# Optimization experiments

Hardware: AMD Instinct MI355X
Metric: run time of the kernel (lower is better)

The kernel has to match this reference:

```python
import jax, jax.numpy as jnp
import numpy as np

N_NODES = 50000
N_EDGES = 800000
D_IN = 128
D_HID = 128
D_OUT = 128
BN_EPS = 1e-5


def _lin_params(key, d_out, d_in, bias=True):
    k1, k2 = jax.random.split(key)
    s = 1.0 / np.sqrt(d_in)
    W = jax.random.uniform(k1, (d_out, d_in), jnp.float32, -s, s)
    b = jax.random.uniform(k2, (d_out,), jnp.float32, -s, s) if bias else None
    return W, b


def setup_inputs() -> dict:
    key = jax.random.key(0)
    ks = jax.random.split(key, 10)
    x = jax.random.normal(ks[0], (N_NODES, D_IN), jnp.float32)
    edge_index = jax.random.randint(ks[1], (2, N_EDGES), 0, N_NODES, jnp.int32)
    Wl0, bl0 = _lin_params(ks[2], D_HID, D_IN)
    Wr0, _ = _lin_params(ks[3], D_HID, D_IN, bias=False)
    Wl1, bl1 = _lin_params(ks[4], D_HID, D_HID)
    Wr1, _ = _lin_params(ks[5], D_HID, D_HID, bias=False)
    Wl2, bl2 = _lin_params(ks[6], D_OUT, D_HID)
    Wr2, _ = _lin_params(ks[7], D_OUT, D_HID, bias=False)
    gamma1 = jnp.ones((D_HID,), jnp.float32)
    beta1 = jnp.zeros((D_HID,), jnp.float32)
    return dict(x=x, edge_index=edge_index,
                Wl0=Wl0, bl0=bl0, Wr0=Wr0,
                Wl1=Wl1, bl1=bl1, Wr1=Wr1,
                Wl2=Wl2, bl2=bl2, Wr2=Wr2,
                gamma1=gamma1, beta1=beta1)


def sage_conv(x, src, dst, Wl, bl, Wr):
    # gather messages from source nodes, mean-aggregate at destination nodes
    msg = x[src]                                                   # [E, d]
    agg = jax.ops.segment_sum(msg, dst, num_segments=N_NODES)      # [N, d]
    cnt = jax.ops.segment_sum(jnp.ones((src.shape[0],), x.dtype), dst,
                              num_segments=N_NODES)
    mean = agg / jnp.maximum(cnt, 1.0)[:, None]
    return mean @ Wl.T + bl + x @ Wr.T


def batch_norm(x, gamma, beta):
    mu = jnp.mean(x, axis=0)
    var = jnp.var(x, axis=0)
    return (x - mu) * jax.lax.rsqrt(var + BN_EPS) * gamma + beta


def reference(x, edge_index, Wl0, bl0, Wr0, Wl1, bl1, Wr1, Wl2, bl2, Wr2,
              gamma1, beta1):
    src, dst = edge_index[0], edge_index[1]
    h = jax.nn.relu(sage_conv(x, src, dst, Wl0, bl0, Wr0))
    h = sage_conv(h, src, dst, Wl1, bl1, Wr1)
    h = jax.nn.relu(batch_norm(h, gamma1, beta1))
    return sage_conv(h, src, dst, Wl2, bl2, Wr2)
```

## Files before the change

### kernel.cpp

```cpp
#include <hip/hip_runtime.h>
#include <hip/hip_bf16.h>
#include <cstdint>

#define N_NODES 50000
#define N_EDGES 800000
#define D 128
#define NBUCK 196
#define CAP 4608

typedef __attribute__((ext_vector_type(4))) float f32x4;
typedef __attribute__((ext_vector_type(8))) short s16x8;

__device__ __forceinline__ float bflo(uint32_t v) { return __uint_as_float(v << 16); }
__device__ __forceinline__ float bfhi(uint32_t v) { return __uint_as_float(v & 0xffff0000u); }
__device__ __forceinline__ uint32_t f2b(float f) {
    uint32_t x = __float_as_uint(f);
    uint32_t r = x + 0x7fffu + ((x >> 16) & 1u);
    return r >> 16;
}
__device__ __forceinline__ uint32_t pack2(float lo, float hi) {
    return f2b(lo) | (f2b(hi) << 16);
}

__global__ void prep_k(const float* __restrict__ x,
                       const float* __restrict__ Wl0, const float* __restrict__ Wr0,
                       const float* __restrict__ Wl1, const float* __restrict__ Wr1,
                       const float* __restrict__ Wl2, const float* __restrict__ Wr2,
                       uint32_t* __restrict__ X0, uint32_t* __restrict__ Wc)
{
    const int NX = N_NODES * D / 2;
    const int NW = 3 * 128 * 128;
    for (int i = blockIdx.x * blockDim.x + threadIdx.x; i < NX + NW;
         i += gridDim.x * blockDim.x) {
        if (i < NX) {
            const float2 v = reinterpret_cast<const float2*>(x)[i];
            X0[i] = pack2(v.x, v.y);
        } else {
            int j = i - NX;
            int l = j / 16384;
            int r = j % 16384;
            int n = r >> 7;
            int k2 = (r & 127) * 2;
            const float* Wl = (l == 0) ? Wl0 : (l == 1) ? Wl1 : Wl2;
            const float* Wr = (l == 0) ? Wr0 : (l == 1) ? Wr1 : Wr2;
            float a, b;
            if (k2 < 128) { a = Wl[n * 128 + k2];       b = Wl[n * 128 + k2 + 1]; }
            else          { a = Wr[n * 128 + k2 - 128]; b = Wr[n * 128 + k2 - 127]; }
            Wc[j] = pack2(a, b);
        }
    }
}

__global__ __launch_bounds__(256) void bucket_k(const int* __restrict__ src,
                                                const int* __restrict__ dst,
                                                int* __restrict__ bcnt,
                                                uint2* __restrict__ ebuf)
{
    __shared__ int h[256], base[256], cur[256];
    const int t = threadIdx.x;
    h[t] = 0; cur[t] = 0;
    __syncthreads();
    const int chunk = (N_EDGES + gridDim.x - 1) / gridDim.x;
    const int e0 = blockIdx.x * chunk;
    int e1 = e0 + chunk; if (e1 > N_EDGES) e1 = N_EDGES;
    for (int e = e0 + t; e < e1; e += 256) {
        int b = dst[e] >> 8;
        atomicAdd(&h[b], 1);
    }
    __syncthreads();
    if (t < NBUCK) base[t] = (h[t] > 0) ? atomicAdd(&bcnt[t], h[t]) : 0;
    __syncthreads();
    for (int e = e0 + t; e < e1; e += 256) {
        int s = src[e], d = dst[e];
        int b = d >> 8;
        int r = atomicAdd(&cur[b], 1);
        int pos = base[b] + r;
        if (pos < CAP) ebuf[b * CAP + pos] = make_uint2((uint32_t)s, (uint32_t)d);
    }
}

__global__ void bscan_k(const int* __restrict__ bcnt, int* __restrict__ bbase) {
    __shared__ int s[256];
    int t = threadIdx.x;
    int v = (t < NBUCK) ? bcnt[t] : 0;
    s[t] = v;
    __syncthreads();
    for (int d = 1; d < 256; d <<= 1) {
        int tmp = (t >= d) ? s[t - d] : 0;
        __syncthreads();
        s[t] += tmp;
        __syncthreads();
    }
    if (t < NBUCK) bbase[t] = s[t] - v;
}

__global__ __launch_bounds__(256) void csr_k(const uint2* __restrict__ ebuf,
                                             const int* __restrict__ bcnt,
                                             const int* __restrict__ bbase,
                                             int* __restrict__ rowptr,
                                             int* __restrict__ adj)
{
    __shared__ int cntL[256], offL[256], curL[256];
    const int b = blockIdx.x;
    const int t = threadIdx.x;
    const int n0 = b << 8;
    const int m = bcnt[b];
    const int gbase = bbase[b];
    cntL[t] = 0; curL[t] = 0;
    __syncthreads();
    const uint2* eb = ebuf + b * CAP;
    for (int i = t; i < m; i += 256)
        atomicAdd(&cntL[(int)eb[i].y - n0], 1);
    __syncthreads();
    int v = cntL[t];
    offL[t] = v;
    __syncthreads();
    for (int d = 1; d < 256; d <<= 1) {
        int tmp = (t >= d) ? offL[t - d] : 0;
        __syncthreads();
        offL[t] += tmp;
        __syncthreads();
    }
    int excl = offL[t] - v;
    int node = n0 + t;
    if (node < N_NODES) rowptr[node] = gbase + excl;
    if (b == NBUCK - 1 && t == 0) rowptr[N_NODES] = N_EDGES;
    __syncthreads();
    offL[t] = excl;
    __syncthreads();
    for (int i = t; i < m; i += 256) {
        uint2 e = eb[i];
        int d = (int)e.y - n0;
        int r = atomicAdd(&curL[d], 1);
        adj[gbase + offL[d] + r] = (int)e.x;
    }
}

__global__ __launch_bounds__(256) void agg_k(const uint32_t* __restrict__ inB,
                                             const int* __restrict__ rowptr,
                                             const int* __restrict__ adj,
                                             uint32_t* __restrict__ meanb)
{
    const int wid = threadIdx.x >> 6;
    const int lane = threadIdx.x & 63;
    const int n = blockIdx.x * 4 + wid;
    if (n >= N_NODES) return;
    const int start = rowptr[n], end = rowptr[n + 1];
    const int sub = lane >> 4;
    const int col4 = lane & 15;

    float acc[8];
#pragma unroll
    for (int k = 0; k < 8; ++k) acc[k] = 0.f;

    for (int base = start; base < end; base += 64) {
        int cnt = end - base;
        if (cnt > 64) cnt = 64;
        int idx = (base + lane < end) ? adj[base + lane] : 0;
        for (int j = 0; j < cnt; j += 8) {
            int e0 = j + sub;
            int e1 = j + 4 + sub;
            int s0 = __shfl(idx, e0, 64);
            int s1 = __shfl(idx, e1, 64);
            bool v0 = e0 < cnt;
            bool v1 = e1 < cnt;
            uint4 a = *reinterpret_cast<const uint4*>(inB + (v0 ? s0 : 0) * 64 + col4 * 4);
            uint4 b = *reinterpret_cast<const uint4*>(inB + (v1 ? s1 : 0) * 64 + col4 * 4);
            if (!v0) a = make_uint4(0, 0, 0, 0);
            if (!v1) b = make_uint4(0, 0, 0, 0);
            acc[0] += bflo(a.x); acc[1] += bfhi(a.x);
            acc[2] += bflo(a.y); acc[3] += bfhi(a.y);
            acc[4] += bflo(a.z); acc[5] += bfhi(a.z);
            acc[6] += bflo(a.w); acc[7] += bfhi(a.w);
            acc[0] += bflo(b.x); acc[1] += bfhi(b.x);
            acc[2] += bflo(b.y); acc[3] += bfhi(b.y);
            acc[4] += bflo(b.z); acc[5] += bfhi(b.z);
            acc[6] += bflo(b.w); acc[7] += bfhi(b.w);
        }
    }

#pragma unroll
    for (int k = 0; k < 8; ++k) {
        acc[k] += __shfl_xor(acc[k], 16, 64);
        acc[k] += __shfl_xor(acc[k], 32, 64);
    }

    if (sub == 0) {
        int deg = end - start;
        float sc = 1.0f / (float)(deg > 0 ? deg : 1);
        uint4 w;
        w.x = pack2(acc[0] * sc, acc[1] * sc);
        w.y = pack2(acc[2] * sc, acc[3] * sc);
        w.z = pack2(acc[4] * sc, acc[5] * sc);
        w.w = pack2(acc[6] * sc, acc[7] * sc);
        *reinterpret_cast<uint4*>(meanb + n * 64 + col4 * 4) = w;
    }
}

template <int LAYER>
__global__ __launch_bounds__(256) void gemm_k(const uint32_t* __restrict__ meanb,
                                              const uint32_t* __restrict__ inB,
                                              const uint32_t* __restrict__ Wc,
                                              const float* __restrict__ bias,
                                              void* __restrict__ outp)
{
    __shared__ uint32_t Bs[16384];
    const int t = threadIdx.x;
    const uint32_t* Wg = Wc + LAYER * 16384;
    {
        const int r = t >> 1;
        const int h = t & 1;
        const int sw = (r & 7) << 2;
#pragma unroll
        for (int q = 0; q < 16; ++q) {
            int off = h * 64 + q * 4;
            *reinterpret_cast<uint4*>(Bs + r * 128 + (off ^ sw)) =
                *reinterpret_cast<const uint4*>(Wg + r * 128 + off);
        }
    }
    __syncthreads();

    const int lane = t & 63;
    const int wid = t >> 6;
    const int rowBase = blockIdx.x * 128 + wid * 32;
    const int l15 = lane & 15;
    const int kc = lane >> 4;
    int m0 = rowBase + l15;
    int m1 = m0 + 16;
    int m0c = m0 < N_NODES ? m0 : N_NODES - 1;
    int m1c = m1 < N_NODES ? m1 : N_NODES - 1;

    f32x4 acc[2][8];
#pragma unroll
    for (int a = 0; a < 2; ++a)
#pragma unroll
        for (int b = 0; b < 8; ++b) acc[a][b] = (f32x4){0.f, 0.f, 0.f, 0.f};

#pragma unroll
    for (int ks = 0; ks < 8; ++ks) {
        const uint32_t* Asrc = (ks < 4) ? meanb : inB;
        const int koff = (ks & 3) * 16 + kc * 4;
        s16x8 a0 = *reinterpret_cast<const s16x8*>(Asrc + m0c * 64 + koff);
        s16x8 a1 = *reinterpret_cast<const s16x8*>(Asrc + m1c * 64 + koff);
#pragma unroll
        for (int nf = 0; nf < 8; ++nf) {
            const int row = nf * 16 + l15;
            const int off = (ks * 16 + kc * 4) ^ ((row & 7) << 2);
            s16x8 b = *reinterpret_cast<const s16x8*>(Bs + row * 128 + off);
            acc[0][nf] = __builtin_amdgcn_mfma_f32_16x16x32_bf16(a0, b, acc[0][nf], 0, 0, 0);
            acc[1][nf] = __builtin_amdgcn_mfma_f32_16x16x32_bf16(a1, b, acc[1][nf], 0, 0, 0);
        }
    }

    const int rb = rowBase + (lane >> 4) * 4;
#pragma unroll
    for (int mf = 0; mf < 2; ++mf) {
#pragma unroll
        for (int nf = 0; nf < 8; ++nf) {
            int col = nf * 16 + l15;
            float bia = bias[col];
#pragma unroll
            for (int r = 0; r < 4; ++r) {
                int row = rb + mf * 16 + r;
                if (row < N_NODES) {
                    float v = acc[mf][nf][r] + bia;
                    if (LAYER == 0) v = v > 0.f ? v : 0.f;
                    if (LAYER == 2)
                        ((float*)outp)[row * 128 + col] = v;
                    else
                        ((unsigned short*)outp)[row * 128 + col] = (unsigned short)f2b(v);
                }
            }
        }
    }
}

__global__ void bn_stats_k(const uint32_t* __restrict__ G2, float* __restrict__ colsums) {
    __shared__ float4 red[256];
    int c2 = threadIdx.x & 63;
    int rg = threadIdx.x >> 6;
    float s0 = 0, q0 = 0, s1 = 0, q1 = 0;
    for (int r = blockIdx.x * 4 + rg; r < N_NODES; r += gridDim.x * 4) {
        uint32_t v = G2[r * 64 + c2];
        float f0 = bflo(v), f1 = bfhi(v);
        s0 += f0; q0 += f0 * f0;
        s1 += f1; q1 += f1 * f1;
    }
    red[threadIdx.x] = make_float4(s0, q0, s1, q1);
    __syncthreads();
    if (threadIdx.x < 64) {
        float4 a = red[threadIdx.x], b = red[threadIdx.x + 64];
        float4 c = red[threadIdx.x + 128], d = red[threadIdx.x + 192];
        atomicAdd(&colsums[c2 * 2],       a.x + b.x + c.x + d.x);
        atomicAdd(&colsums[c2 * 2 + 1],   a.z + b.z + c.z + d.z);
        atomicAdd(&colsums[128 + c2 * 2],     a.y + b.y + c.y + d.y);
        atomicAdd(&colsums[128 + c2 * 2 + 1], a.w + b.w + c.w + d.w);
    }
}

__global__ void bn_final_k(const float* __restrict__ colsums, const float* __restrict__ gamma,
                           const float* __restrict__ beta, float* __restrict__ bnp) {
    int c = threadIdx.x;
    float mu = colsums[c] / (float)N_NODES;
    float var = colsums[128 + c] / (float)N_NODES - mu * mu;
    float sc = gamma[c] * rsqrtf(var + 1e-5f);
    bnp[c] = sc;
    bnp[128 + c] = beta[c] - mu * sc;
}

__global__ void bn_apply_k(const uint32_t* __restrict__ G2, const float* __restrict__ bnp,
                           uint32_t* __restrict__ H2) {
    const int total = N_NODES * 64;
    for (int i = blockIdx.x * blockDim.x + threadIdx.x; i < total;
         i += gridDim.x * blockDim.x) {
        int c = (i & 63) * 2;
        uint32_t v = G2[i];
        float f0 = bflo(v) * bnp[c] + bnp[128 + c];
        float f1 = bfhi(v) * bnp[c + 1] + bnp[128 + c + 1];
        f0 = f0 > 0.f ? f0 : 0.f;
        f1 = f1 > 0.f ? f1 : 0.f;
        H2[i] = pack2(f0, f1);
    }
}

extern "C" void kernel_launch(void* const* d_in, const int* in_sizes, int n_in,
                              void* d_out, int out_size, void* d_ws, size_t ws_size,
                              hipStream_t stream)
{
    const float* x      = (const float*)d_in[0];
    const int*   ei     = (const int*)d_in[1];
    const float* Wl0    = (const float*)d_in[2];
    const float* bl0    = (const float*)d_in[3];
    const float* Wr0    = (const float*)d_in[4];
    const float* Wl1    = (const float*)d_in[5];
    const float* bl1    = (const float*)d_in[6];
    const float* Wr1    = (const float*)d_in[7];
    const float* Wl2    = (const float*)d_in[8];
    const float* bl2    = (const float*)d_in[9];
    const float* Wr2    = (const float*)d_in[10];
    const float* gamma1 = (const float*)d_in[11];
    const float* beta1  = (const float*)d_in[12];

    char* ws = (char*)d_ws;
    int*      bcnt    = (int*)(ws + 0);
    float*    colsums = (float*)(ws + 1024);
    int*      bbase   = (int*)(ws + 2048);
    int*      rowptr  = (int*)(ws + 4096);
    int*      adj     = (int*)(ws + 204160);
    uint2*    ebuf    = (uint2*)(ws + 3404160);
    uint32_t* bufA    = (uint32_t*)(ws + 10629504);
    uint32_t* bufB    = (uint32_t*)(ws + 23429504);
    uint32_t* bufC    = (uint32_t*)(ws + 36229504);
    uint32_t* Wc      = (uint32_t*)(ws + 49029504);
    float*    bnp     = (float*)(ws + 49226112);
    uint32_t* X0 = bufA;
    uint32_t* MB = bufB;
    uint32_t* G1 = bufC;
    uint32_t* G2 = bufA;
    uint32_t* H2 = bufC;

    const int* srcI = ei;
    const int* dstI = ei + N_EDGES;

    hipMemsetAsync(ws, 0, 2048, stream);
    prep_k<<<2048, 256, 0, stream>>>(x, Wl0, Wr0, Wl1, Wr1, Wl2, Wr2, X0, Wc);
    bucket_k<<<512, 256, 0, stream>>>(srcI, dstI, bcnt, ebuf);
    bscan_k<<<1, 256, 0, stream>>>(bcnt, bbase);
    csr_k<<<NBUCK, 256, 0, stream>>>(ebuf, bcnt, bbase, rowptr, adj);

    agg_k<<<12500, 256, 0, stream>>>(X0, rowptr, adj, MB);
    gemm_k<0><<<391, 256, 0, stream>>>(MB, X0, Wc, bl0, (void*)G1);
    agg_k<<<12500, 256, 0, stream>>>(G1, rowptr, adj, MB);
    gemm_k<1><<<391, 256, 0, stream>>>(MB, G1, Wc, bl1, (void*)G2);
    bn_stats_k<<<512, 256, 0, stream>>>(G2, colsums);
    bn_final_k<<<1, 128, 0, stream>>>(colsums, gamma1, beta1, bnp);
    bn_apply_k<<<2048, 256, 0, stream>>>(G2, bnp, H2);
    agg_k<<<12500, 256, 0, stream>>>(H2, rowptr, adj, MB);
    gemm_k<2><<<391, 256, 0, stream>>>(MB, H2, Wc, bl2, d_out);
}
```

Measured before the change: 306.2 us.

## Fuse preprocessing and bucketing, fold scan into CSR, fuse batch-norm into GEMM/aggregation

Merges the weight/feature conversion and the edge-bucketing kernels into one launch, and moves the bucket prefix scan into each CSR block. BN statistics are now accumulated in the layer-1 GEMM epilogue using shared-memory atomics. The normalize-plus-ReLU step is applied on the fly in the layer-2 aggregation gather and in the layer-2 GEMM's root-feature load, which removes the separate stats, finalize and apply passes and the H2 buffer. The cost is extra FMA and max work per gathered element in aggregation (about 16 neighbor reads per node), redundant scans in every CSR block, and statistics computed from fp32 values before bf16 rounding.

```diff
diff --git a/kernel.cpp b/kernel.cpp
--- a/kernel.cpp
+++ b/kernel.cpp
@@ -22,90 +22,81 @@
     return f2b(lo) | (f2b(hi) << 16);
 }
 
-__global__ void prep_k(const float* __restrict__ x,
+__global__ __launch_bounds__(256) void pb_k(const float* __restrict__ x,
                        const float* __restrict__ Wl0, const float* __restrict__ Wr0,
                        const float* __restrict__ Wl1, const float* __restrict__ Wr1,
                        const float* __restrict__ Wl2, const float* __restrict__ Wr2,
-                       uint32_t* __restrict__ X0, uint32_t* __restrict__ Wc)
+                       uint32_t* __restrict__ X0, uint32_t* __restrict__ Wc,
+                       const int* __restrict__ src, const int* __restrict__ dst,
+                       int* __restrict__ bcnt, uint2* __restrict__ ebuf)
 {
-    const int NX = N_NODES * D / 2;
-    const int NW = 3 * 128 * 128;
-    for (int i = blockIdx.x * blockDim.x + threadIdx.x; i < NX + NW;
-         i += gridDim.x * blockDim.x) {
-        if (i < NX) {
-            const float2 v = reinterpret_cast<const float2*>(x)[i];
-            X0[i] = pack2(v.x, v.y);
-        } else {
-            int j = i - NX;
-            int l = j / 16384;
-            int r = j % 16384;
-            int n = r >> 7;
-            int k2 = (r & 127) * 2;
-            const float* Wl = (l == 0) ? Wl0 : (l == 1) ? Wl1 : Wl2;
-            const float* Wr = (l == 0) ? Wr0 : (l == 1) ? Wr1 : Wr2;
-            float a, b;
-            if (k2 < 128) { a = Wl[n * 128 + k2];       b = Wl[n * 128 + k2 + 1]; }
-            else          { a = Wr[n * 128 + k2 - 128]; b = Wr[n * 128 + k2 - 127]; }
-            Wc[j] = pack2(a, b);
-        }
-    }
-}
-
-__global__ __launch_bounds__(256) void bucket_k(const int* __restrict__ src,
-                                                const int* __restrict__ dst,
-                                                int* __restrict__ bcnt,
-                                                uint2* __restrict__ ebuf)
-{
-    __shared__ int h[256], base[256], cur[256];
     const int t = threadIdx.x;
-    h[t] = 0; cur[t] = 0;
-    __syncthreads();
-    const int chunk = (N_EDGES + gridDim.x - 1) / gridDim.x;
-    const int e0 = blockIdx.x * chunk;
-    int e1 = e0 + chunk; if (e1 > N_EDGES) e1 = N_EDGES;
-    for (int e = e0 + t; e < e1; e += 256) {
-        int b = dst[e] >> 8;
-        atomicAdd(&h[b], 1);
-    }
-    __syncthreads();
-    if (t < NBUCK) base[t] = (h[t] > 0) ? atomicAdd(&bcnt[t], h[t]) : 0;
-    __syncthreads();
-    for (int e = e0 + t; e < e1; e += 256) {
-        int s = src[e], d = dst[e];
-        int b = d >> 8;
-        int r = atomicAdd(&cur[b], 1);
-        int pos = base[b] + r;
-        if (pos < CAP) ebuf[b * CAP + pos] = make_uint2((uint32_t)s, (uint32_t)d);
-    }
-}
-
-__global__ void bscan_k(const int* __restrict__ bcnt, int* __restrict__ bbase) {
-    __shared__ int s[256];
-    int t = threadIdx.x;
-    int v = (t < NBUCK) ? bcnt[t] : 0;
-    s[t] = v;
-    __syncthreads();
-    for (int d = 1; d < 256; d <<= 1) {
-        int tmp = (t >= d) ? s[t - d] : 0;
-        __syncthreads();
-        s[t] += tmp;
-        __syncthreads();
-    }
-    if (t < NBUCK) bbase[t] = s[t] - v;
+    if (blockIdx.x < 512) {
+        __shared__ int h[256], base[256], cur[256];
+        h[t] = 0; cur[t] = 0;
+        __syncthreads();
+        const int chunk = (N_EDGES + 511) / 512;
+        const int e0 = blockIdx.x * chunk;
+        int e1 = e0 + chunk; if (e1 > N_EDGES) e1 = N_EDGES;
+        for (int e = e0 + t; e < e1; e += 256) {
+            int b = dst[e] >> 8;
+            atomicAdd(&h[b], 1);
+        }
+        __syncthreads();
+        if (t < NBUCK) base[t] = (h[t] > 0) ? atomicAdd(&bcnt[t], h[t]) : 0;
+        __syncthreads();
+        for (int e = e0 + t; e < e1; e += 256) {
+            int s = src[e], d = dst[e];
+            int b = d >> 8;
+            int r = atomicAdd(&cur[b], 1);
+            int pos = base[b] + r;
+            if (pos < CAP) ebuf[b * CAP + pos] = make_uint2((uint32_t)s, (uint32_t)d);
+        }
+    } else {
+        const int NX = N_NODES * D / 2;
+        const int NW = 3 * 128 * 128;
+        const int bid = blockIdx.x - 512;
+        for (int i = bid * 256 + t; i < NX + NW; i += 2048 * 256) {
+            if (i < NX) {
+                const float2 v = reinterpret_cast<const float2*>(x)[i];
+                X0[i] = pack2(v.x, v.y);
+            } else {
+                int j = i - NX;
+                int l = j / 16384;
+                int r = j % 16384;
+                int n = r >> 7;
+                int k2 = (r & 127) * 2;
+                const float* Wl = (l == 0) ? Wl0 : (l == 1) ? Wl1 : Wl2;
+                const float* Wr = (l == 0) ? Wr0 : (l == 1) ? Wr1 : Wr2;
+                float a, b;
+                if (k2 < 128) { a = Wl[n * 128 + k2];       b = Wl[n * 128 + k2 + 1]; }
+                else          { a = Wr[n * 128 + k2 - 128]; b = Wr[n * 128 + k2 - 127]; }
+                Wc[j] = pack2(a, b);
+            }
+        }
+    }
 }
 
 __global__ __launch_bounds__(256) void csr_k(const uint2* __restrict__ ebuf,
                                              const int* __restrict__ bcnt,
-                                             const int* __restrict__ bbase,
                                              int* __restrict__ rowptr,
                                              int* __restrict__ adj)
 {
-    __shared__ int cntL[256], offL[256], curL[256];
+    __shared__ int bs[256], cntL[256], offL[256], curL[256];
     const int b = blockIdx.x;
     const int t = threadIdx.x;
     const int n0 = b << 8;
+    int bv = (t < NBUCK) ? bcnt[t] : 0;
+    bs[t] = bv;
+    __syncthreads();
+    for (int d = 1; d < 256; d <<= 1) {
+        int tmp = (t >= d) ? bs[t - d] : 0;
+        __syncthreads();
+        bs[t] += tmp;
+        __syncthreads();
+    }
+    const int gbase = (b == 0) ? 0 : bs[b - 1];
     const int m = bcnt[b];
-    const int gbase = bbase[b];
     cntL[t] = 0; curL[t] = 0;
     __syncthreads();
     const uint2* eb = ebuf + b * CAP;
@@ -136,19 +127,42 @@
     }
 }
 
+template <int APPLYBN>
 __global__ __launch_bounds__(256) void agg_k(const uint32_t* __restrict__ inB,
                                              const int* __restrict__ rowptr,
                                              const int* __restrict__ adj,
-                                             uint32_t* __restrict__ meanb)
+                                             uint32_t* __restrict__ meanb,
+                                             const float* __restrict__ colsums,
+                                             const float* __restrict__ gamma,
+                                             const float* __restrict__ beta)
 {
     const int wid = threadIdx.x >> 6;
     const int lane = threadIdx.x & 63;
     const int n = blockIdx.x * 4 + wid;
-    if (n >= N_NODES) return;
-    const int start = rowptr[n], end = rowptr[n + 1];
     const int sub = lane >> 4;
     const int col4 = lane & 15;
 
+    float vsc[8], vsh[8];
+    if constexpr (APPLYBN) {
+        __shared__ float bnS[256];
+        const int t = threadIdx.x;
+        if (t < 128) {
+            float mu  = colsums[t] * (1.0f / N_NODES);
+            float var = colsums[128 + t] * (1.0f / N_NODES) - mu * mu;
+            float sc  = gamma[t] * rsqrtf(var + 1e-5f);
+            bnS[t] = sc;
+            bnS[128 + t] = beta[t] - mu * sc;
+        }
+        __syncthreads();
+#pragma unroll
+        for (int k = 0; k < 8; ++k) {
+            int c = col4 * 8 + k;
+            vsc[k] = bnS[c]; vsh[k] = bnS[128 + c];
+        }
+    }
+    if (n >= N_NODES) return;
+
+    const int start = rowptr[n], end = rowptr[n + 1];
     float acc[8];
 #pragma unroll
     for (int k = 0; k < 8; ++k) acc[k] = 0.f;
@@ -166,16 +180,28 @@
             bool v1 = e1 < cnt;
             uint4 a = *reinterpret_cast<const uint4*>(inB + (v0 ? s0 : 0) * 64 + col4 * 4);
             uint4 b = *reinterpret_cast<const uint4*>(inB + (v1 ? s1 : 0) * 64 + col4 * 4);
-            if (!v0) a = make_uint4(0, 0, 0, 0);
-            if (!v1) b = make_uint4(0, 0, 0, 0);
-            acc[0] += bflo(a.x); acc[1] += bfhi(a.x);
-            acc[2] += bflo(a.y); acc[3] += bfhi(a.y);
-            acc[4] += bflo(a.z); acc[5] += bfhi(a.z);
-            acc[6] += bflo(a.w); acc[7] += bfhi(a.w);
-            acc[0] += bflo(b.x); acc[1] += bfhi(b.x);
-            acc[2] += bflo(b.y); acc[3] += bfhi(b.y);
-            acc[4] += bflo(b.z); acc[5] += bfhi(b.z);
-            acc[6] += bflo(b.w); acc[7] += bfhi(b.w);
+            if constexpr (APPLYBN) {
+                float m0 = v0 ? 1.f : 0.f;
+                float m1 = v1 ? 1.f : 0.f;
+#define ACCBN(K, GA, GB) acc[K] += m0 * fmaxf(fmaf((GA), vsc[K], vsh[K]), 0.f) \
+                                 + m1 * fmaxf(fmaf((GB), vsc[K], vsh[K]), 0.f)
+                ACCBN(0, bflo(a.x), bflo(b.x)); ACCBN(1, bfhi(a.x), bfhi(b.x));
+                ACCBN(2, bflo(a.y), bflo(b.y)); ACCBN(3, bfhi(a.y), bfhi(b.y));
+                ACCBN(4, bflo(a.z), bflo(b.z)); ACCBN(5, bfhi(a.z), bfhi(b.z));
+                ACCBN(6, bflo(a.w), bflo(b.w)); ACCBN(7, bfhi(a.w), bfhi(b.w));
+#undef ACCBN
+            } else {
+                if (!v0) a = make_uint4(0, 0, 0, 0);
+                if (!v1) b = make_uint4(0, 0, 0, 0);
+                acc[0] += bflo(a.x); acc[1] += bfhi(a.x);
+                acc[2] += bflo(a.y); acc[3] += bfhi(a.y);
+                acc[4] += bflo(a.z); acc[5] += bfhi(a.z);
+                acc[6] += bflo(a.w); acc[7] += bfhi(a.w);
+                acc[0] += bflo(b.x); acc[1] += bfhi(b.x);
+                acc[2] += bflo(b.y); acc[3] += bfhi(b.y);
+                acc[4] += bflo(b.z); acc[5] += bfhi(b.z);
+                acc[6] += bflo(b.w); acc[7] += bfhi(b.w);
+            }
         }
     }
 
@@ -197,14 +223,32 @@
     }
 }
 
+__device__ __forceinline__ s16x8 bn8(uint4 u, const float* bnS, int cb) {
+    uint32_t uu[4] = {u.x, u.y, u.z, u.w};
+    uint32_t w[4];
+#pragma unroll
+    for (int i = 0; i < 4; ++i) {
+        int c = cb + 2 * i;
+        float lo = fmaxf(fmaf(bflo(uu[i]), bnS[c],     bnS[128 + c]),     0.f);
+        float hi = fmaxf(fmaf(bfhi(uu[i]), bnS[c + 1], bnS[128 + c + 1]), 0.f);
+        w[i] = pack2(lo, hi);
+    }
+    uint4 r = make_uint4(w[0], w[1], w[2], w[3]);
+    return __builtin_bit_cast(s16x8, r);
+}
+
 template <int LAYER>
 __global__ __launch_bounds__(256) void gemm_k(const uint32_t* __restrict__ meanb,
                                               const uint32_t* __restrict__ inB,
                                               const uint32_t* __restrict__ Wc,
                                               const float* __restrict__ bias,
-                                              void* __restrict__ outp)
+                                              void* __restrict__ outp,
+                                              float* __restrict__ colsums,
+                                              const float* __restrict__ gamma,
+                                              const float* __restrict__ beta)
 {
     __shared__ uint32_t Bs[16384];
+    __shared__ float extraS[256];
     const int t = threadIdx.x;
     const uint32_t* Wg = Wc + LAYER * 16384;
     {
@@ -216,6 +260,18 @@
             int off = h * 64 + q * 4;
             *reinterpret_cast<uint4*>(Bs + r * 128 + (off ^ sw)) =
                 *reinterpret_cast<const uint4*>(Wg + r * 128 + off);
+        }
+    }
+    if constexpr (LAYER == 1) {
+        extraS[t] = 0.f;
+    }
+    if constexpr (LAYER == 2) {
+        if (t < 128) {
+            float mu  = colsums[t] * (1.0f / N_NODES);
+            float var = colsums[128 + t] * (1.0f / N_NODES) - mu * mu;
+            float sc  = gamma[t] * rsqrtf(var + 1e-5f);
+            extraS[t] = sc;
+            extraS[128 + t] = beta[t] - mu * sc;
         }
     }
     __syncthreads();
@@ -238,10 +294,23 @@
 
 #pragma unroll
     for (int ks = 0; ks < 8; ++ks) {
-        const uint32_t* Asrc = (ks < 4) ? meanb : inB;
         const int koff = (ks & 3) * 16 + kc * 4;
-        s16x8 a0 = *reinterpret_cast<const s16x8*>(Asrc + m0c * 64 + koff);
-        s16x8 a1 = *reinterpret_cast<const s16x8*>(Asrc + m1c * 64 + koff);
+        s16x8 a0, a1;
+        if (ks < 4) {
+            a0 = *reinterpret_cast<const s16x8*>(meanb + m0c * 64 + koff);
+            a1 = *reinterpret_cast<const s16x8*>(meanb + m1c * 64 + koff);
+        } else {
+            if constexpr (LAYER == 2) {
+                const int cb = (ks & 3) * 32 + kc * 8;
+                uint4 u0 = *reinterpret_cast<const uint4*>(inB + m0c * 64 + koff);
+                uint4 u1 = *reinterpret_cast<const uint4*>(inB + m1c * 64 + koff);
+                a0 = bn8(u0, extraS, cb);
+                a1 = bn8(u1, extraS, cb);
+            } else {
+                a0 = *reinterpret_cast<const s16x8*>(inB + m0c * 64 + koff);
+                a1 = *reinterpret_cast<const s16x8*>(inB + m1c * 64 + koff);
+            }
+        }
 #pragma unroll
         for (int nf = 0; nf < 8; ++nf) {
             const int row = nf * 16 + l15;
@@ -254,11 +323,12 @@
 
     const int rb = rowBase + (lane >> 4) * 4;
 #pragma unroll
-    for (int mf = 0; mf < 2; ++mf) {
-#pragma unroll
-        for (int nf = 0; nf < 8; ++nf) {
-            int col = nf * 16 + l15;
-            float bia = bias[col];
+    for (int nf = 0; nf < 8; ++nf) {
+        int col = nf * 16 + l15;
+        float bia = bias[col];
+        float s = 0.f, q = 0.f;
+#pragma unroll
+        for (int mf = 0; mf < 2; ++mf) {
 #pragma unroll
             for (int r = 0; r < 4; ++r) {
                 int row = rb + mf * 16 + r;
@@ -269,57 +339,21 @@
                         ((float*)outp)[row * 128 + col] = v;
                     else
                         ((unsigned short*)outp)[row * 128 + col] = (unsigned short)f2b(v);
+                    if constexpr (LAYER == 1) { s += v; q += v * v; }
                 }
             }
         }
-    }
-}
-
-__global__ void bn_stats_k(const uint32_t* __restrict__ G2, float* __restrict__ colsums) {
-    __shared__ float4 red[256];
-    int c2 = threadIdx.x & 63;
-    int rg = threadIdx.x >> 6;
-    float s0 = 0, q0 = 0, s1 = 0, q1 = 0;
-    for (int r = blockIdx.x * 4 + rg; r < N_NODES; r += gridDim.x * 4) {
-        uint32_t v = G2[r * 64 + c2];
-        float f0 = bflo(v), f1 = bfhi(v);
-        s0 += f0; q0 += f0 * f0;
-        s1 += f1; q1 += f1 * f1;
-    }
-    red[threadIdx.x] = make_float4(s0, q0, s1, q1);
-    __syncthreads();
-    if (threadIdx.x < 64) {
-        float4 a = red[threadIdx.x], b = red[threadIdx.x + 64];
-        float4 c = red[threadIdx.x + 128], d = red[threadIdx.x + 192];
-        atomicAdd(&colsums[c2 * 2],       a.x + b.x + c.x + d.x);
-        atomicAdd(&colsums[c2 * 2 + 1],   a.z + b.z + c.z + d.z);
-        atomicAdd(&colsums[128 + c2 * 2],     a.y + b.y + c.y + d.y);
-        atomicAdd(&colsums[128 + c2 * 2 + 1], a.w + b.w + c.w + d.w);
-    }
-}
-
-__global__ void bn_final_k(const float* __restrict__ colsums, const float* __restrict__ gamma,
-                           const float* __restrict__ beta, float* __restrict__ bnp) {
-    int c = threadIdx.x;
-    float mu = colsums[c] / (float)N_NODES;
-    float var = colsums[128 + c] / (float)N_NODES - mu * mu;
-    float sc = gamma[c] * rsqrtf(var + 1e-5f);
-    bnp[c] = sc;
-    bnp[128 + c] = beta[c] - mu * sc;
-}
-
-__global__ void bn_apply_k(const uint32_t* __restrict__ G2, const float* __restrict__ bnp,
-                           uint32_t* __restrict__ H2) {
-    const int total = N_NODES * 64;
-    for (int i = blockIdx.x * blockDim.x + threadIdx.x; i < total;
-         i += gridDim.x * blockDim.x) {
-        int c = (i & 63) * 2;
-        uint32_t v = G2[i];
-        float f0 = bflo(v) * bnp[c] + bnp[128 + c];
-        float f1 = bfhi(v) * bnp[c + 1] + bnp[128 + c + 1];
-        f0 = f0 > 0.f ? f0 : 0.f;
-        f1 = f1 > 0.f ? f1 : 0.f;
-        H2[i] = pack2(f0, f1);
+        if constexpr (LAYER == 1) {
+            atomicAdd(&extraS[col], s);
+            atomicAdd(&extraS[128 + col], q);
+        }
+    }
+    if constexpr (LAYER == 1) {
+        __syncthreads();
+        if (t < 128) {
+            atomicAdd(&colsums[t], extraS[t]);
+            atomicAdd(&colsums[128 + t], extraS[128 + t]);
+        }
     }
 }
 
@@ -344,7 +378,6 @@
     char* ws = (char*)d_ws;
     int*      bcnt    = (int*)(ws + 0);
     float*    colsums = (float*)(ws + 1024);
-    int*      bbase   = (int*)(ws + 2048);
     int*      rowptr  = (int*)(ws + 4096);
     int*      adj     = (int*)(ws + 204160);
     uint2*    ebuf    = (uint2*)(ws + 3404160);
@@ -352,29 +385,23 @@
     uint32_t* bufB    = (uint32_t*)(ws + 23429504);
     uint32_t* bufC    = (uint32_t*)(ws + 36229504);
     uint32_t* Wc      = (uint32_t*)(ws + 49029504);
-    float*    bnp     = (float*)(ws + 49226112);
     uint32_t* X0 = bufA;
     uint32_t* MB = bufB;
     uint32_t* G1 = bufC;
     uint32_t* G2 = bufA;
-    uint32_t* H2 = bufC;
 
     const int* srcI = ei;
     const int* dstI = ei + N_EDGES;
 
     hipMemsetAsync(ws, 0, 2048, stream);
-    prep_k<<<2048, 256, 0, stream>>>(x, Wl0, Wr0, Wl1, Wr1, Wl2, Wr2, X0, Wc);
-    bucket_k<<<512, 256, 0, stream>>>(srcI, dstI, bcnt, ebuf);
-    bscan_k<<<1, 256, 0, stream>>>(bcnt, bbase);
-    csr_k<<<NBUCK, 256, 0, stream>>>(ebuf, bcnt, bbase, rowptr, adj);
-
-    agg_k<<<12500, 256, 0, stream>>>(X0, rowptr, adj, MB);
-    gemm_k<0><<<391, 256, 0, stream>>>(MB, X0, Wc, bl0, (void*)G1);
-    agg_k<<<12500, 256, 0, stream>>>(G1, rowptr, adj, MB);
-    gemm_k<1><<<391, 256, 0, stream>>>(MB, G1, Wc, bl1, (void*)G2);
-    bn_stats_k<<<512, 256, 0, stream>>>(G2, colsums);
-    bn_final_k<<<1, 128, 0, stream>>>(colsums, gamma1, beta1, bnp);
-    bn_apply_k<<<2048, 256, 0, stream>>>(G2, bnp, H2);
-    agg_k<<<12500, 256, 0, stream>>>(H2, rowptr, adj, MB);
-    gemm_k<2><<<391, 256, 0, stream>>>(MB, H2, Wc, bl2, d_out);
-}
+    pb_k<<<2560, 256, 0, stream>>>(x, Wl0, Wr0, Wl1, Wr1, Wl2, Wr2, X0, Wc,
+                                   srcI, dstI, bcnt, ebuf);
+    csr_k<<<NBUCK, 256, 0, stream>>>(ebuf, bcnt, rowptr, adj);
+
+    agg_k<0><<<12500, 256, 0, stream>>>(X0, rowptr, adj, MB, nullptr, nullptr, nullptr);
+    gemm_k<0><<<391, 256, 0, stream>>>(MB, X0, Wc, bl0, (void*)G1, nullptr, nullptr, nullptr);
+    agg_k<0><<<12500, 256, 0, stream>>>(G1, rowptr, adj, MB, nullptr, nullptr, nullptr);
+    gemm_k<1><<<391, 256, 0, stream>>>(MB, G1, Wc, bl1, (void*)G2, colsums, nullptr, nullptr);
+    agg_k<1><<<12500, 256, 0, stream>>>(G2, rowptr, adj, MB, colsums, gamma1, beta1);
+    gemm_k<2><<<391, 256, 0, stream>>>(MB, G2, Wc, bl2, d_out, colsums, gamma1, beta1);
+}
```

Result: faster. 281.6 us (-8.0%).
